# Optimization experiments

Hardware: AMD Instinct MI355X
Metric: run time of the kernel (lower is better)

The kernel has to match this reference:

```python
import jax, jax.numpy as jnp
import numpy as np

K = 36  # neighbors

def _gather(points, idx):
    # points: [B,N,C], idx: [B,N,K] -> [B,N,K,C]
    return jax.vmap(lambda p, i: p[i])(points, idx)

def setup_inputs() -> dict:
    key = jax.random.key(0)
    ks = jax.random.split(key, 16)
    B, N, d_points, d_model = 4, 4096, 32, 128
    def lin(k, fan_in, shape):
        return jax.random.normal(k, shape, dtype=jnp.float32) / np.sqrt(fan_in)
    return {
        "features": jax.random.normal(ks[0], (B, N, d_points), dtype=jnp.float32),
        "xyz": jax.random.uniform(ks[1], (B, N, 3), dtype=jnp.float32),
        "W1": lin(ks[2], d_points, (d_model, d_points)), "b1": jnp.zeros((d_model,), jnp.float32),
        "W2": lin(ks[3], d_model, (d_model, d_model)), "b2": jnp.zeros((d_model,), jnp.float32),
        "Wd1": lin(ks[4], 3, (d_model, 3)), "bd1": jnp.zeros((d_model,), jnp.float32),
        "Wd2": lin(ks[5], d_model, (d_model, d_model)), "bd2": jnp.zeros((d_model,), jnp.float32),
        "Wg1": lin(ks[6], d_model, (d_model, d_model)), "bg1": jnp.zeros((d_model,), jnp.float32),
        "Wg2": lin(ks[7], d_model, (d_model, d_model)), "bg2": jnp.zeros((d_model,), jnp.float32),
    }

def reference(features, xyz, W1, b1, W2, b2, Wd1, bd1, Wd2, bd2, Wg1, bg1, Wg2, bg2):
    # square_distance: [B,N,N]
    sq = jnp.sum(xyz * xyz, axis=-1)
    dists = sq[:, :, None] + sq[:, None, :] - 2.0 * jnp.einsum('bnc,bmc->bnm', xyz, xyz)
    knn_idx = jnp.argsort(dists, axis=-1)[:, :, :K]            # [B,N,K]
    knn_xyz = _gather(xyz, knn_idx)                             # [B,N,K,3]
    x = features @ W1.T + b1                                    # [B,N,d]
    k = _gather(x, knn_idx)                                     # [B,N,K,d]
    v = k
    # fc_delta(xyz[:,:,None] - knn_xyz)
    d_in = xyz[:, :, None, :] - knn_xyz                         # [B,N,K,3]
    pos_enc = jax.nn.relu(d_in @ Wd1.T + bd1) @ Wd2.T + bd2     # [B,N,K,d]
    # fc_gamma(q[:,:,None] - k + pos_enc)
    g_in = x[:, :, None, :] - k + pos_enc
    attn_pre = jax.nn.relu(g_in @ Wg1.T + bg1) @ Wg2.T + bg2    # [B,N,K,d]
    attn = jax.nn.softmax(attn_pre / np.sqrt(x.shape[-1]).astype(np.float32), axis=-2)
    res = jnp.einsum('bmnf,bmnf->bmf', attn, v + pos_enc)       # [B,N,d]
    res = res @ W2.T + b2 + x
    return (res, attn)
```

## Files before the change

### kernel.cpp

```cpp
#include <hip/hip_runtime.h>
#include <math.h>

#define BB 4
#define NPT 4096
#define DP 32
#define DD 128
#define KNB 36

typedef unsigned short ushort_t;
typedef unsigned int uint_t;
typedef unsigned long long ull;
typedef __attribute__((ext_vector_type(8))) short bf16x8;
typedef __attribute__((ext_vector_type(4))) float f32x4;
typedef __attribute__((ext_vector_type(4))) uint_t u32x4;

__device__ __forceinline__ ushort_t f2bf(float f) {
    unsigned u = __float_as_uint(f);
    unsigned r = (u + 0x7FFFu + ((u >> 16) & 1u)) >> 16;
    return (ushort_t)r;
}
__device__ __forceinline__ uint_t cvtpk(float lo, float hi) {
    uint_t r;
    asm("v_cvt_pk_bf16_f32 %0, %1, %2" : "=v"(r) : "v"(lo), "v"(hi));
    return r;
}
__device__ __forceinline__ ushort_t f2bf1(float f) { return (ushort_t)cvtpk(f, f); }
__device__ __forceinline__ float bf2f(ushort_t h) {
    return __uint_as_float((unsigned)h << 16);
}
__device__ __forceinline__ int swzi(int r, int f) {
    return (r << 7) + (((f >> 3) ^ (r & 15)) << 3) + (f & 7);
}

__global__ __launch_bounds__(256) void k_wcvt(const float* __restrict__ Wd2,
                                              const float* __restrict__ Wg1,
                                              const float* __restrict__ Wg2,
                                              const float* __restrict__ W2,
                                              ushort_t* __restrict__ wb) {
    int i = blockIdx.x * 256 + threadIdx.x;
    wb[i]           = f2bf(Wd2[i]);
    wb[i + 16384]   = f2bf(Wg1[i]);
    wb[i + 32768]   = f2bf(Wg2[i]);
    wb[i + 49152]   = f2bf(W2[i]);
}

__global__ __launch_bounds__(128) void k_x(const float* __restrict__ feat,
                                           const float* __restrict__ xyz,
                                           const float* __restrict__ W1,
                                           const float* __restrict__ b1,
                                           float* __restrict__ x,
                                           float* __restrict__ sq) {
    int row = blockIdx.x;
    int t = threadIdx.x;
    __shared__ float sf[DP];
    if (t < DP) sf[t] = feat[row * DP + t];
    __syncthreads();
    float acc = 0.f;
#pragma unroll
    for (int c = 0; c < DP; ++c) acc = fmaf(sf[c], W1[t * DP + c], acc);
    x[(size_t)row * DD + t] = acc + b1[t];
    if (t == 0) {
        float a = xyz[row * 3 + 0], b = xyz[row * 3 + 1], c = xyz[row * 3 + 2];
        float s = __fadd_rn(__fadd_rn(__fmul_rn(a, a), __fmul_rn(b, b)),
                            __fmul_rn(c, c));
        sq[row] = s;
    }
}

__global__ __launch_bounds__(256) void k_knn2(const float* __restrict__ xyz,
                                              const float* __restrict__ sq,
                                              int* __restrict__ knn) {
    const int row = blockIdx.x;
    const int b = row >> 12;
    const int t = threadIdx.x;
    const int lane = t & 63, wv = t >> 6;

    __shared__ __align__(16) ull cand[2048];
    __shared__ int wsum[4];
    __shared__ ull wred[4];
    __shared__ ull sbest;
    __shared__ int sC, sCnt;

    uint_t* hist4 = (uint_t*)cand;

    const float qx = xyz[row * 3 + 0], qy = xyz[row * 3 + 1], qz = xyz[row * 3 + 2];
    const float qs = sq[row];
    const float* bx = xyz + (size_t)b * NPT * 3;
    const float* bs = sq + (size_t)b * NPT;

#pragma unroll
    for (int i = 0; i < 16; ++i) hist4[t + (i << 8)] = 0;
    if (t == 0) sCnt = 0;
    __syncthreads();

    uint_t k16[16];
#pragma unroll
    for (int i = 0; i < 16; ++i) {
        int m = t + (i << 8);
        float px = bx[m * 3 + 0], py = bx[m * 3 + 1], pz = bx[m * 3 + 2];
        float d0 = __fmul_rn(qx, px);
        float d1 = __fmaf_rn(qy, py, d0);
        float dot = __fmaf_rn(qz, pz, d1);
        float d = __fsub_rn(__fadd_rn(qs, bs[m]), __fmul_rn(2.0f, dot));
        unsigned u = __float_as_uint(d);
        u = (u & 0x80000000u) ? ~u : (u | 0x80000000u);
        k16[i] = u;
        int bin = (u < 0x80000000u) ? 0 : (int)((u - 0x80000000u) >> 21);
        atomicAdd(&hist4[(bin << 2) | (t & 3)], 1u);
    }
    __syncthreads();

    int s_t = 0;
#pragma unroll
    for (int i = 0; i < 16; ++i) s_t += (int)hist4[(t << 4) + i];
    int v = s_t;
    for (int off = 1; off < 64; off <<= 1) {
        int o = __shfl_up(v, off, 64);
        if (lane >= off) v += o;
    }
    if (lane == 63) wsum[wv] = v;
    __syncthreads();
    int base = 0;
    for (int w0 = 0; w0 < wv; ++w0) base += wsum[w0];
    int cumIncl = base + v, cumExcl = cumIncl - s_t;
    if (cumExcl < KNB && cumIncl >= KNB) {
        int run = cumExcl;
#pragma unroll
        for (int j = 0; j < 4; ++j) {
            int bb = (t << 2) + j;
            int h = (int)(hist4[(bb << 2) + 0] + hist4[(bb << 2) + 1] +
                          hist4[(bb << 2) + 2] + hist4[(bb << 2) + 3]);
            if (run + h >= KNB) { sC = bb; break; }
            run += h;
        }
    }
    __syncthreads();
    const int C = sC;

#pragma unroll
    for (int i = 0; i < 16; ++i) {
        uint_t u = k16[i];
        int bin = (u < 0x80000000u) ? 0 : (int)((u - 0x80000000u) >> 21);
        if (bin <= C) {
            int p = atomicAdd(&sCnt, 1);
            if (p < 2048) cand[p] = ((ull)u << 32) | (uint_t)(t + (i << 8));
        }
    }
    __syncthreads();
    const int cnt = sCnt;

    if (cnt <= 64) {
        if (wv == 0) {
            ull x = (lane < cnt) ? cand[lane] : ~0ull;
#pragma unroll
            for (int k = 2; k <= 64; k <<= 1) {
#pragma unroll
                for (int j = k >> 1; j > 0; j >>= 1) {
                    ull o = __shfl_xor(x, j, 64);
                    bool up = ((lane & k) == 0);
                    bool lower = ((lane & j) == 0);
                    ull mn = (x < o) ? x : o;
                    ull mx = (x < o) ? o : x;
                    x = (up == lower) ? mn : mx;
                }
            }
            if (lane < KNB) knn[(size_t)row * KNB + lane] = (int)(x & 0xffffffffu);
        }
        return;
    }

    if (cnt <= 2048) {
        ull lk = ~0ull;
        for (int i = t; i < cnt; i += 256) { ull k = cand[i]; if (k < lk) lk = k; }
        for (int r = 0; r < KNB; ++r) {
            ull k = lk;
#pragma unroll
            for (int off = 32; off >= 1; off >>= 1) {
                ull o = __shfl_down(k, off, 64);
                if (o < k) k = o;
            }
            if (lane == 0) wred[wv] = k;
            __syncthreads();
            if (t == 0) {
                ull best = wred[0];
                for (int w0 = 1; w0 < 4; ++w0) if (wred[w0] < best) best = wred[w0];
                sbest = best;
                knn[(size_t)row * KNB + r] = (int)(best & 0xffffffffu);
            }
            __syncthreads();
            ull best = sbest;
            if (lk == best) {
                for (int i = t; i < cnt; i += 256)
                    if (cand[i] == best) cand[i] = ~0ull;
                ull nm = ~0ull;
                for (int i = t; i < cnt; i += 256) { ull kk = cand[i]; if (kk < nm) nm = kk; }
                lk = nm;
            }
        }
        return;
    }

    {
        uint_t* bm = (uint_t*)cand;
        if (t < 128) bm[t] = 0;
        __syncthreads();
        ull lk = ~0ull;
#pragma unroll
        for (int i = 0; i < 16; ++i) {
            ull k = ((ull)k16[i] << 32) | (uint_t)(t + (i << 8));
            if (k < lk) lk = k;
        }
        for (int r = 0; r < KNB; ++r) {
            ull k = lk;
#pragma unroll
            for (int off = 32; off >= 1; off >>= 1) {
                ull o = __shfl_down(k, off, 64);
                if (o < k) k = o;
            }
            if (lane == 0) wred[wv] = k;
            __syncthreads();
            if (t == 0) {
                ull best = wred[0];
                for (int w0 = 1; w0 < 4; ++w0) if (wred[w0] < best) best = wred[w0];
                sbest = best;
                knn[(size_t)row * KNB + r] = (int)(best & 0xffffffffu);
            }
            __syncthreads();
            ull best = sbest;
            int bi = (int)(best & 0xffffffffu);
            if ((bi & 255) == t) {
                bm[bi >> 5] |= (1u << (bi & 31));
                ull nm = ~0ull;
#pragma unroll
                for (int i = 0; i < 16; ++i) {
                    int m = t + (i << 8);
                    if ((bm[m >> 5] >> (m & 31)) & 1u) continue;
                    ull kk = ((ull)k16[i] << 32) | (uint_t)m;
                    if (kk < nm) nm = kk;
                }
                lk = nm;
            }
        }
    }
}

__global__ __launch_bounds__(256) void k_fused2(
    const float* __restrict__ xyz, const float* __restrict__ x,
    const int* __restrict__ knn,
    const float* __restrict__ Wd1, const float* __restrict__ bd1,
    const float* __restrict__ bd2, const float* __restrict__ bg1,
    const float* __restrict__ bg2, const float* __restrict__ b2,
    const ushort_t* __restrict__ Wd2b, const ushort_t* __restrict__ Wg1b,
    const ushort_t* __restrict__ Wg2b, const ushort_t* __restrict__ W2b,
    float* __restrict__ out_res, float* __restrict__ out_attn) {

    const int p0 = blockIdx.x * 4;
    const int b = p0 >> 12;
    const int t = threadIdx.x;
    const int w = t >> 6;
    const int l = t & 63;

    __shared__ __align__(16) ushort_t Abuf[144 * 128];
    __shared__ __align__(16) ushort_t Vbuf[144 * 128];
    __shared__ int sidxb[144];
    __shared__ float dxb[144 * 3];
    __shared__ float Wd1s[384];
    __shared__ float bd1s[128];

    const int c0 = ((w * 2) << 4) + (l & 15);
    const int c1 = c0 + 16;
    float xn_r[2][4];
#pragma unroll
    for (int g = 0; g < 4; ++g) {
        xn_r[0][g] = x[(size_t)(p0 + g) * DD + c0];
        xn_r[1][g] = x[(size_t)(p0 + g) * DD + c1];
    }
    const float bd2_r[2] = {bd2[c0], bd2[c1]};
    const float bg1_r[2] = {bg1[c0], bg1[c1]};
    const float bg2_r[2] = {bg2[c0], bg2[c1]};
    const float b2_r[2]  = {b2[c0],  b2[c1]};

    if (t < 144) sidxb[t] = knn[(size_t)p0 * KNB + t];
    if (t < 128) bd1s[t] = bd1[t];
    if (t >= 128 && t < 128 + 96) {
        int i = t - 128;
        reinterpret_cast<float4*>(Wd1s)[i] = reinterpret_cast<const float4*>(Wd1)[i];
    }
    __syncthreads();

    if (t < 144) {
        int g = (t * 456) >> 14;
        int j = sidxb[t];
#pragma unroll
        for (int c = 0; c < 3; ++c)
            dxb[t * 3 + c] = xyz[(size_t)(p0 + g) * 3 + c] - xyz[((size_t)(b << 12) + j) * 3 + c];
    }
    for (int e = t; e < 144 * 16; e += 256) {
        int r = e >> 4, cb = e & 15;
        const float4* xr = reinterpret_cast<const float4*>(x + ((size_t)(b << 12) + sidxb[r]) * DD);
        float4 a0 = xr[cb * 2], a1 = xr[cb * 2 + 1];
        u32x4 pk = {cvtpk(a0.x, a0.y), cvtpk(a0.z, a0.w),
                    cvtpk(a1.x, a1.y), cvtpk(a1.z, a1.w)};
        *reinterpret_cast<u32x4*>(&Vbuf[(r << 7) + ((cb ^ (r & 15)) << 3)]) = pk;
    }
    __syncthreads();

    for (int e = t; e < 144 * 16; e += 256) {
        int r = e >> 4, cb = e & 15;
        float dx0 = dxb[r * 3 + 0], dx1 = dxb[r * 3 + 1], dx2 = dxb[r * 3 + 2];
        float v[8];
#pragma unroll
        for (int u = 0; u < 8; ++u) {
            int f = (cb << 3) + u;
            v[u] = fmaxf(fmaf(Wd1s[f * 3 + 0], dx0,
                         fmaf(Wd1s[f * 3 + 1], dx1,
                              Wd1s[f * 3 + 2] * dx2)) + bd1s[f], 0.f);
        }
        u32x4 pk = {cvtpk(v[0], v[1]), cvtpk(v[2], v[3]),
                    cvtpk(v[4], v[5]), cvtpk(v[6], v[7])};
        *reinterpret_cast<u32x4*>(&Abuf[(r << 7) + ((cb ^ (r & 15)) << 3)]) = pk;
    }
    __syncthreads();

    const f32x4 z4 = {0.f, 0.f, 0.f, 0.f};

    auto run_gemm = [&](const ushort_t* Wb, f32x4 acc[9][2]) {
        bf16x8 bfrag[2][4];
#pragma unroll
        for (int n2 = 0; n2 < 2; ++n2)
#pragma unroll
            for (int kt = 0; kt < 4; ++kt) {
                int f = ((w * 2 + n2) << 4) + (l & 15);
                int k = (kt << 5) + ((l >> 4) << 3);
                bfrag[n2][kt] = *reinterpret_cast<const bf16x8*>(Wb + f * 128 + k);
            }
        __builtin_amdgcn_s_setprio(1);
#pragma unroll
        for (int mt = 0; mt < 9; ++mt) {
#pragma unroll
            for (int kt = 0; kt < 4; ++kt) {
                int r = (mt << 4) + (l & 15);
                int cs = ((kt << 2) + (l >> 4)) ^ (l & 15);
                bf16x8 a = *reinterpret_cast<const bf16x8*>(&Abuf[(r << 7) + (cs << 3)]);
                acc[mt][0] = __builtin_amdgcn_mfma_f32_16x16x32_bf16(a, bfrag[0][kt], acc[mt][0], 0, 0, 0);
                acc[mt][1] = __builtin_amdgcn_mfma_f32_16x16x32_bf16(a, bfrag[1][kt], acc[mt][1], 0, 0, 0);
            }
        }
        __builtin_amdgcn_s_setprio(0);
    };

    {
        f32x4 acc[9][2];
#pragma unroll
        for (int mt = 0; mt < 9; ++mt) { acc[mt][0] = z4; acc[mt][1] = z4; }
        run_gemm(Wd2b, acc);
        __syncthreads();
#pragma unroll
        for (int mt = 0; mt < 9; ++mt)
#pragma unroll
            for (int n2 = 0; n2 < 2; ++n2) {
                int col = (n2 == 0) ? c0 : c1;
#pragma unroll
                for (int rr = 0; rr < 4; ++rr) {
                    int row = (mt << 4) + ((l >> 4) << 2) + rr;
                    int g = (row * 456) >> 14;
                    int vs = swzi(row, col);
                    float pe = acc[mt][n2][rr] + bd2_r[n2];
                    float xk = bf2f(Vbuf[vs]);
                    Vbuf[vs] = f2bf1(xk + pe);
                    float gin = (xn_r[n2][g] - xk) + pe;
                    Abuf[swzi(row, col)] = f2bf1(gin);
                }
            }
        __syncthreads();
    }

    {
        f32x4 acc[9][2];
#pragma unroll
        for (int mt = 0; mt < 9; ++mt) { acc[mt][0] = z4; acc[mt][1] = z4; }
        run_gemm(Wg1b, acc);
        __syncthreads();
#pragma unroll
        for (int mt = 0; mt < 9; ++mt)
#pragma unroll
            for (int n2 = 0; n2 < 2; ++n2) {
                int col = (n2 == 0) ? c0 : c1;
#pragma unroll
                for (int rr = 0; rr < 4; ++rr) {
                    int row = (mt << 4) + ((l >> 4) << 2) + rr;
                    Abuf[swzi(row, col)] = f2bf1(fmaxf(acc[mt][n2][rr] + bg1_r[n2], 0.f));
                }
            }
        __syncthreads();
    }

    {
        f32x4 acc[9][2];
#pragma unroll
        for (int mt = 0; mt < 9; ++mt) { acc[mt][0] = z4; acc[mt][1] = z4; }
        run_gemm(Wg2b, acc);
        __syncthreads();
#pragma unroll
        for (int mt = 0; mt < 9; ++mt)
#pragma unroll
            for (int n2 = 0; n2 < 2; ++n2) {
                int col = (n2 == 0) ? c0 : c1;
#pragma unroll
                for (int rr = 0; rr < 4; ++rr) {
                    int row = (mt << 4) + ((l >> 4) << 2) + rr;
                    Abuf[swzi(row, col)] = f2bf1(acc[mt][n2][rr] + bg2_r[n2]);
                }
            }
        __syncthreads();
    }

    const float sc = 0.08838834764831845f;
    const int f = t & 127;
    const int gA = t >> 7, gB = gA + 2;

    auto softmax_pv = [&](int g) -> float {
        int r0 = g * KNB;
        float p[KNB];
        float m = -__builtin_inff();
#pragma unroll
        for (int kk = 0; kk < KNB; ++kk) {
            p[kk] = bf2f(Abuf[swzi(r0 + kk, f)]);
            m = fmaxf(m, p[kk]);
        }
        float sum = 0.f;
#pragma unroll
        for (int kk = 0; kk < KNB; ++kk) {
            float e_ = __expf((p[kk] - m) * sc);
            p[kk] = e_;
            sum += e_;
        }
        float inv = 1.f / sum;
        float ra = 0.f;
        size_t obase = ((size_t)(p0 + g) * KNB) * DD + f;
#pragma unroll
        for (int kk = 0; kk < KNB; ++kk) {
            float a_ = p[kk] * inv;
            out_attn[obase + (size_t)kk * DD] = a_;
            ra = fmaf(a_, bf2f(Vbuf[swzi(r0 + kk, f)]), ra);
        }
        return ra;
    };
    float raA = softmax_pv(gA);
    float raB = softmax_pv(gB);
    __syncthreads();
    Abuf[swzi(gA, f)] = f2bf1(raA);
    Abuf[swzi(gB, f)] = f2bf1(raB);
    __syncthreads();

    {
        f32x4 acc0 = z4, acc1 = z4;
#pragma unroll
        for (int kt = 0; kt < 4; ++kt) {
            int r = (l & 15);
            int cs = ((kt << 2) + (l >> 4)) ^ (l & 15);
            bf16x8 a = *reinterpret_cast<const bf16x8*>(&Abuf[(r << 7) + (cs << 3)]);
            int k = (kt << 5) + ((l >> 4) << 3);
            bf16x8 b0 = *reinterpret_cast<const bf16x8*>(W2b + c0 * 128 + k);
            bf16x8 b1 = *reinterpret_cast<const bf16x8*>(W2b + c1 * 128 + k);
            acc0 = __builtin_amdgcn_mfma_f32_16x16x32_bf16(a, b0, acc0, 0, 0, 0);
            acc1 = __builtin_amdgcn_mfma_f32_16x16x32_bf16(a, b1, acc1, 0, 0, 0);
        }
        if ((l >> 4) == 0) {
#pragma unroll
            for (int rr = 0; rr < 4; ++rr) {
                out_res[(size_t)(p0 + rr) * DD + c0] = acc0[rr] + b2_r[0] + xn_r[0][rr];
                out_res[(size_t)(p0 + rr) * DD + c1] = acc1[rr] + b2_r[1] + xn_r[1][rr];
            }
        }
    }
}

extern "C" void kernel_launch(void* const* d_in, const int* in_sizes, int n_in,
                              void* d_out, int out_size, void* d_ws, size_t ws_size,
                              hipStream_t stream) {
    const float* feat = (const float*)d_in[0];
    const float* xyz = (const float*)d_in[1];
    const float* W1 = (const float*)d_in[2];
    const float* b1 = (const float*)d_in[3];
    const float* W2 = (const float*)d_in[4];
    const float* b2 = (const float*)d_in[5];
    const float* Wd1 = (const float*)d_in[6];
    const float* bd1 = (const float*)d_in[7];
    const float* Wd2 = (const float*)d_in[8];
    const float* bd2 = (const float*)d_in[9];
    const float* Wg1 = (const float*)d_in[10];
    const float* bg1 = (const float*)d_in[11];
    const float* Wg2 = (const float*)d_in[12];
    const float* bg2 = (const float*)d_in[13];

    float* out = (float*)d_out;
    float* out_res = out;
    float* out_attn = out + (size_t)BB * NPT * DD;

    float* ws_x = (float*)d_ws;
    float* ws_sq = ws_x + (size_t)BB * NPT * DD;
    int* ws_idx = (int*)(ws_sq + (size_t)BB * NPT);
    ushort_t* wb = (ushort_t*)(ws_idx + (size_t)BB * NPT * KNB);
    ushort_t* Wd2b = wb;
    ushort_t* Wg1b = wb + 16384;
    ushort_t* Wg2b = wb + 32768;
    ushort_t* W2b = wb + 49152;

    hipLaunchKernelGGL(k_wcvt, dim3(64), dim3(256), 0, stream, Wd2, Wg1, Wg2, W2, wb);
    hipLaunchKernelGGL(k_x, dim3(BB * NPT), dim3(128), 0, stream,
                       feat, xyz, W1, b1, ws_x, ws_sq);
    hipLaunchKernelGGL(k_knn2, dim3(BB * NPT), dim3(256), 0, stream,
                       xyz, ws_sq, ws_idx);
    hipLaunchKernelGGL(k_fused2, dim3(BB * NPT / 4), dim3(256), 0, stream,
                       xyz, ws_x, ws_idx, Wd1, bd1, bd2, bg1, bg2, b2,
                       Wd2b, Wg1b, Wg2b, W2b, out_res, out_attn);
}
```

Before: 340.8 us.

## Fuse softmax and PV reduction into MFMA accumulator registers, drop LDS round trip

The last gamma GEMM's accumulators now go straight into the softmax: max and sum over the 36 neighbors are done in registers, with cross-lane shuffles standing in for the round trip through shared memory. The v+pos_enc values are kept packed as bf16 in registers from the first epilogue instead of being written back to Vbuf, and attention weights are written and accumulated from the MFMA layout. This removes LDS writes and reads plus a barrier, but raises register pressure (extra packed values per thread). It also changes the attn store pattern from coalesced per-row to 4-row strided per-lane writes.

```diff
diff --git a/kernel.cpp b/kernel.cpp
--- a/kernel.cpp
+++ b/kernel.cpp
@@ -28,6 +28,8 @@
 __device__ __forceinline__ float bf2f(ushort_t h) {
     return __uint_as_float((unsigned)h << 16);
 }
+__device__ __forceinline__ float pk_lo(uint_t u) { return __uint_as_float(u << 16); }
+__device__ __forceinline__ float pk_hi(uint_t u) { return __uint_as_float(u & 0xFFFF0000u); }
 __device__ __forceinline__ int swzi(int r, int f) {
     return (r << 7) + (((f >> 3) ^ (r & 15)) << 3) + (f & 7);
 }
@@ -259,6 +261,7 @@
     const int t = threadIdx.x;
     const int w = t >> 6;
     const int l = t & 63;
+    const int q4 = l >> 4;
 
     __shared__ __align__(16) ushort_t Abuf[144 * 128];
     __shared__ __align__(16) ushort_t Vbuf[144 * 128];
@@ -349,6 +352,8 @@
         __builtin_amdgcn_s_setprio(0);
     };
 
+    uint_t vpe_pk[9][2][2];
+
     {
         f32x4 acc[9][2];
 #pragma unroll
@@ -356,22 +361,27 @@
         run_gemm(Wd2b, acc);
         __syncthreads();
 #pragma unroll
-        for (int mt = 0; mt < 9; ++mt)
+        for (int mt = 0; mt < 9; ++mt) {
+            const int S0 = 4 * mt, G0 = S0 / 9, G1 = (S0 + 3) / 9, TH = 9 * G1 - S0;
 #pragma unroll
             for (int n2 = 0; n2 < 2; ++n2) {
                 int col = (n2 == 0) ? c0 : c1;
+                float xn_sel = (G0 == G1) ? xn_r[n2][G0]
+                                          : ((q4 >= TH) ? xn_r[n2][G1] : xn_r[n2][G0]);
+                float vp[4];
 #pragma unroll
                 for (int rr = 0; rr < 4; ++rr) {
-                    int row = (mt << 4) + ((l >> 4) << 2) + rr;
-                    int g = (row * 456) >> 14;
-                    int vs = swzi(row, col);
+                    int row = (mt << 4) + (q4 << 2) + rr;
                     float pe = acc[mt][n2][rr] + bd2_r[n2];
-                    float xk = bf2f(Vbuf[vs]);
-                    Vbuf[vs] = f2bf1(xk + pe);
-                    float gin = (xn_r[n2][g] - xk) + pe;
+                    float xk = bf2f(Vbuf[swzi(row, col)]);
+                    vp[rr] = xk + pe;
+                    float gin = (xn_sel - xk) + pe;
                     Abuf[swzi(row, col)] = f2bf1(gin);
                 }
-            }
+                vpe_pk[mt][n2][0] = cvtpk(vp[0], vp[1]);
+                vpe_pk[mt][n2][1] = cvtpk(vp[2], vp[3]);
+            }
+        }
         __syncthreads();
     }
 
@@ -388,69 +398,146 @@
                 int col = (n2 == 0) ? c0 : c1;
 #pragma unroll
                 for (int rr = 0; rr < 4; ++rr) {
-                    int row = (mt << 4) + ((l >> 4) << 2) + rr;
+                    int row = (mt << 4) + (q4 << 2) + rr;
                     Abuf[swzi(row, col)] = f2bf1(fmaxf(acc[mt][n2][rr] + bg1_r[n2], 0.f));
                 }
             }
         __syncthreads();
     }
 
+    const float sc = 0.08838834764831845f;
+    const float NEGINF = -__builtin_inff();
+    float ra[4][2];
     {
         f32x4 acc[9][2];
 #pragma unroll
         for (int mt = 0; mt < 9; ++mt) { acc[mt][0] = z4; acc[mt][1] = z4; }
         run_gemm(Wg2b, acc);
-        __syncthreads();
+
 #pragma unroll
         for (int mt = 0; mt < 9; ++mt)
 #pragma unroll
+            for (int n2 = 0; n2 < 2; ++n2)
+#pragma unroll
+                for (int rr = 0; rr < 4; ++rr)
+                    acc[mt][n2][rr] += bg2_r[n2];
+
+        float m[4][2];
+#pragma unroll
+        for (int g = 0; g < 4; ++g) { m[g][0] = NEGINF; m[g][1] = NEGINF; }
+#pragma unroll
+        for (int mt = 0; mt < 9; ++mt) {
+            const int S0 = 4 * mt, G0 = S0 / 9, G1 = (S0 + 3) / 9, TH = 9 * G1 - S0;
+#pragma unroll
+            for (int n2 = 0; n2 < 2; ++n2) {
+                float v = fmaxf(fmaxf(acc[mt][n2][0], acc[mt][n2][1]),
+                                fmaxf(acc[mt][n2][2], acc[mt][n2][3]));
+                if (G0 == G1) {
+                    m[G0][n2] = fmaxf(m[G0][n2], v);
+                } else {
+                    bool hi = (q4 >= TH);
+                    m[G0][n2] = fmaxf(m[G0][n2], hi ? NEGINF : v);
+                    m[G1][n2] = fmaxf(m[G1][n2], hi ? v : NEGINF);
+                }
+            }
+        }
+#pragma unroll
+        for (int g = 0; g < 4; ++g)
+#pragma unroll
+            for (int n2 = 0; n2 < 2; ++n2) {
+                float v = m[g][n2];
+                v = fmaxf(v, __shfl_xor(v, 16, 64));
+                v = fmaxf(v, __shfl_xor(v, 32, 64));
+                m[g][n2] = v;
+            }
+
+        float ssum[4][2];
+#pragma unroll
+        for (int g = 0; g < 4; ++g) { ssum[g][0] = 0.f; ssum[g][1] = 0.f; }
+#pragma unroll
+        for (int mt = 0; mt < 9; ++mt) {
+            const int S0 = 4 * mt, G0 = S0 / 9, G1 = (S0 + 3) / 9, TH = 9 * G1 - S0;
+#pragma unroll
+            for (int n2 = 0; n2 < 2; ++n2) {
+                float mm = (G0 == G1) ? m[G0][n2]
+                                      : ((q4 >= TH) ? m[G1][n2] : m[G0][n2]);
+                float sl = 0.f;
+#pragma unroll
+                for (int rr = 0; rr < 4; ++rr) {
+                    float p = __expf((acc[mt][n2][rr] - mm) * sc);
+                    acc[mt][n2][rr] = p;
+                    sl += p;
+                }
+                if (G0 == G1) {
+                    ssum[G0][n2] += sl;
+                } else {
+                    bool hi = (q4 >= TH);
+                    ssum[G0][n2] += hi ? 0.f : sl;
+                    ssum[G1][n2] += hi ? sl : 0.f;
+                }
+            }
+        }
+        float inv[4][2];
+#pragma unroll
+        for (int g = 0; g < 4; ++g)
+#pragma unroll
+            for (int n2 = 0; n2 < 2; ++n2) {
+                float v = ssum[g][n2];
+                v += __shfl_xor(v, 16, 64);
+                v += __shfl_xor(v, 32, 64);
+                inv[g][n2] = 1.f / v;
+            }
+
+#pragma unroll
+        for (int g = 0; g < 4; ++g) { ra[g][0] = 0.f; ra[g][1] = 0.f; }
+#pragma unroll
+        for (int mt = 0; mt < 9; ++mt) {
+            const int S0 = 4 * mt, G0 = S0 / 9, G1 = (S0 + 3) / 9, TH = 9 * G1 - S0;
+            int g = (G0 == G1) ? G0 : ((q4 >= TH) ? G1 : G0);
+            int j = (S0 + q4) - 9 * g;
+#pragma unroll
             for (int n2 = 0; n2 < 2; ++n2) {
                 int col = (n2 == 0) ? c0 : c1;
-#pragma unroll
-                for (int rr = 0; rr < 4; ++rr) {
-                    int row = (mt << 4) + ((l >> 4) << 2) + rr;
-                    Abuf[swzi(row, col)] = f2bf1(acc[mt][n2][rr] + bg2_r[n2]);
-                }
-            }
-        __syncthreads();
-    }
-
-    const float sc = 0.08838834764831845f;
-    const int f = t & 127;
-    const int gA = t >> 7, gB = gA + 2;
-
-    auto softmax_pv = [&](int g) -> float {
-        int r0 = g * KNB;
-        float p[KNB];
-        float m = -__builtin_inff();
-#pragma unroll
-        for (int kk = 0; kk < KNB; ++kk) {
-            p[kk] = bf2f(Abuf[swzi(r0 + kk, f)]);
-            m = fmaxf(m, p[kk]);
-        }
-        float sum = 0.f;
-#pragma unroll
-        for (int kk = 0; kk < KNB; ++kk) {
-            float e_ = __expf((p[kk] - m) * sc);
-            p[kk] = e_;
-            sum += e_;
-        }
-        float inv = 1.f / sum;
-        float ra = 0.f;
-        size_t obase = ((size_t)(p0 + g) * KNB) * DD + f;
-#pragma unroll
-        for (int kk = 0; kk < KNB; ++kk) {
-            float a_ = p[kk] * inv;
-            out_attn[obase + (size_t)kk * DD] = a_;
-            ra = fmaf(a_, bf2f(Vbuf[swzi(r0 + kk, f)]), ra);
-        }
-        return ra;
-    };
-    float raA = softmax_pv(gA);
-    float raB = softmax_pv(gB);
-    __syncthreads();
-    Abuf[swzi(gA, f)] = f2bf1(raA);
-    Abuf[swzi(gB, f)] = f2bf1(raB);
+                float iv = (G0 == G1) ? inv[G0][n2]
+                                      : ((q4 >= TH) ? inv[G1][n2] : inv[G0][n2]);
+                size_t base = ((size_t)(p0 + g) * KNB + (j << 2)) * DD + col;
+                float v0 = pk_lo(vpe_pk[mt][n2][0]), v1 = pk_hi(vpe_pk[mt][n2][0]);
+                float v2 = pk_lo(vpe_pk[mt][n2][1]), v3 = pk_hi(vpe_pk[mt][n2][1]);
+                float a0 = acc[mt][n2][0] * iv, a1 = acc[mt][n2][1] * iv;
+                float a2 = acc[mt][n2][2] * iv, a3 = acc[mt][n2][3] * iv;
+                out_attn[base]          = a0;
+                out_attn[base + DD]     = a1;
+                out_attn[base + 2 * DD] = a2;
+                out_attn[base + 3 * DD] = a3;
+                float dloc = fmaf(a0, v0, fmaf(a1, v1, fmaf(a2, v2, a3 * v3)));
+                if (G0 == G1) {
+                    ra[G0][n2] += dloc;
+                } else {
+                    bool hi = (q4 >= TH);
+                    ra[G0][n2] += hi ? 0.f : dloc;
+                    ra[G1][n2] += hi ? dloc : 0.f;
+                }
+            }
+        }
+#pragma unroll
+        for (int g = 0; g < 4; ++g)
+#pragma unroll
+            for (int n2 = 0; n2 < 2; ++n2) {
+                float v = ra[g][n2];
+                v += __shfl_xor(v, 16, 64);
+                v += __shfl_xor(v, 32, 64);
+                ra[g][n2] = v;
+            }
+    }
+    __syncthreads();
+
+    if (q4 == 0) {
+#pragma unroll
+        for (int g = 0; g < 4; ++g) {
+            Abuf[swzi(g, c0)] = f2bf1(ra[g][0]);
+            Abuf[swzi(g, c1)] = f2bf1(ra[g][1]);
+        }
+    }
     __syncthreads();
 
     {
```

After: 439.9 us. 1.29x slower.
